# Kernel optimization log

Measured on AMD Instinct MI355X. Metric: run time of the kernel, lower is better.

Reference implementation:

```python
import jax, jax.numpy as jnp
import numpy as np

N = 50000   # nodes
E = 1600000 # edges
NF = 128    # input features
H = 128     # hidden
C = 40      # classes
EPS = 1e-5


def setup_inputs() -> dict:
    key = jax.random.key(0)
    ks = jax.random.split(key, 8)
    s_in = 1.0 / np.sqrt(NF)
    s_h = 1.0 / np.sqrt(H)
    return {
        "x": jax.random.normal(ks[0], (N, NF), jnp.float32),
        "edge_index": jax.random.randint(ks[1], (2, E), 0, N, dtype=jnp.int32),
        "W1": jax.random.normal(ks[2], (NF, H), jnp.float32) * s_in,
        "b1": jnp.zeros((H,), jnp.float32),
        "W2": jax.random.normal(ks[3], (H, H), jnp.float32) * s_h,
        "b2": jnp.zeros((H,), jnp.float32),
        "W3": jax.random.normal(ks[4], (H, H), jnp.float32) * s_h,
        "b3": jnp.zeros((H,), jnp.float32),
        "g1": jnp.ones((H,), jnp.float32), "be1": jnp.zeros((H,), jnp.float32),
        "g2": jnp.ones((H,), jnp.float32), "be2": jnp.zeros((H,), jnp.float32),
        "g3": jnp.ones((H,), jnp.float32), "be3": jnp.zeros((H,), jnp.float32),
        "fcW": jax.random.normal(ks[5], (H, C), jnp.float32) * s_h,
        "fcb": jnp.zeros((C,), jnp.float32),
    }


def _bn(x, g, b):
    # BatchNorm1d training-mode semantics: batch mean / biased batch var
    m = jnp.mean(x, axis=0)
    v = jnp.mean(jnp.square(x - m), axis=0)
    return g * (x - m) * jax.lax.rsqrt(v + EPS) + b


def reference(x, edge_index, W1, b1, W2, b2, W3, b3,
              g1, be1, g2, be2, g3, be3, fcW, fcb):
    n = x.shape[0]
    loop = jnp.arange(n, dtype=edge_index.dtype)
    src = jnp.concatenate([edge_index[0], loop])  # [E+N]
    dst = jnp.concatenate([edge_index[1], loop])
    # symmetric GCN normalization with self-loops
    deg = jax.ops.segment_sum(jnp.ones_like(src, dtype=x.dtype), dst, num_segments=n)
    dis = jnp.where(deg > 0, jax.lax.rsqrt(jnp.maximum(deg, 1.0)), 0.0)
    norm = dis[src] * dis[dst]  # [E+N]

    def conv(h, W, b):
        hw = h @ W  # [n, H]
        msg = hw[src] * norm[:, None]  # [E+N, H] gather + scale
        return jax.ops.segment_sum(msg, dst, num_segments=n) + b  # scatter-add

    h = jax.nn.relu(_bn(conv(x, W1, b1), g1, be1))
    h = jax.nn.relu(_bn(conv(h, W2, b2), g2, be2))  # dropout: eval mode (identity)
    h = jax.nn.relu(_bn(conv(h, W3, b3), g3, be3))
    logits = jax.nn.relu(h @ fcW + fcb)
    return jax.nn.log_softmax(logits, axis=1), logits
```

## Files before the change

### kernel.cpp

```cpp
#include <hip/hip_runtime.h>
#include <hip/hip_bf16.h>
#include <math.h>

#define NODES 50000
#define EDGES 1600000
#define HD    128
#define NC    40
#define EPSV  1e-5f
#define NBKT  196
#define CSRMAX 12032
#define NPART 32

typedef unsigned int uint;
typedef unsigned short ushort;
typedef __attribute__((ext_vector_type(8))) short bfrag;
typedef __attribute__((ext_vector_type(4))) float ffrag;

union FragU { uint4 u; bfrag f; };

__device__ inline ushort bf1(float x) {
  uint u = __float_as_uint(x);
  return (ushort)((u + 0x7fffu + ((u >> 16) & 1u)) >> 16);
}
__device__ inline uint bf2(float a, float b) {
  return (uint)bf1(a) | ((uint)bf1(b) << 16);
}
__device__ inline float ulo(uint u) { return __uint_as_float(u << 16); }
__device__ inline float uhi(uint u) { return __uint_as_float(u & 0xffff0000u); }

__global__ __launch_bounds__(256)
void k_bin_prepw(const int* __restrict__ src, const int* __restrict__ dst,
                 int* __restrict__ bcur, uint* __restrict__ staging, int e_,
                 const float* __restrict__ W1, const float* __restrict__ W2,
                 const float* __restrict__ W3, const float* __restrict__ fcW,
                 ushort* __restrict__ wt) {
  if (blockIdx.x >= 196) {
    int idx = (blockIdx.x - 196) * 256 + threadIdx.x;
    if (idx < 49152) {
      int r = idx >> 14;
      int i = idx & 16383;
      int nn = i >> 7, k = i & 127;
      const float* W = (r == 0) ? W1 : ((r == 1) ? W2 : W3);
      wt[idx] = bf1(W[k * 128 + nn]);
    } else if (idx < 55296) {
      int i = idx - 49152;
      int nn = i >> 7, k = i & 127;
      wt[idx] = (nn < NC) ? bf1(fcW[k * NC + nn]) : (ushort)0;
    }
    return;
  }
  __shared__ uint ent[8192];
  __shared__ int h[256], inc[256], lofs[256], cur[256], gb[256];
  int t = threadIdx.x;
  h[t] = 0;
  __syncthreads();
  int base = blockIdx.x * 8192;
  int cntE = min(8192, e_ - base);
  for (int i = t; i < cntE; i += 256) atomicAdd(&h[dst[base + i] >> 8], 1);
  __syncthreads();
  inc[t] = h[t];
  __syncthreads();
#pragma unroll
  for (int off = 1; off < 256; off <<= 1) {
    int y = (t >= off) ? inc[t - off] : 0;
    __syncthreads();
    inc[t] += y;
    __syncthreads();
  }
  lofs[t] = inc[t] - h[t];
  cur[t] = 0;
  __syncthreads();
  for (int i = t; i < cntE; i += 256) {
    int e = base + i;
    int d = dst[e];
    int b = d >> 8;
    uint en = (uint)(src[e] & 0xffff) | ((uint)(d & 255) << 16) | ((uint)b << 24);
    int p = lofs[b] + atomicAdd(&cur[b], 1);
    ent[p] = en;
  }
  __syncthreads();
  if (h[t]) gb[t] = atomicAdd(&bcur[t], h[t]);
  __syncthreads();
  for (int i = t; i < cntE; i += 256) {
    uint en = ent[i];
    int b = en >> 24;
    staging[(size_t)b * CSRMAX + gb[b] + (i - lofs[b])] = en;
  }
}

__global__ __launch_bounds__(256)
void k_csr(const uint* __restrict__ staging, const int* __restrict__ bcur,
           ushort* __restrict__ csr, int2* __restrict__ row_se,
           float* __restrict__ dis, int n) {
  __shared__ uint ent[CSRMAX];
  __shared__ ushort srt[CSRMAX];
  __shared__ int cnt_[256], ofs_[256], cur_[256];
  int b = blockIdx.x, t = threadIdx.x;
  size_t base = (size_t)b * CSRMAX;
  int cnt = min(bcur[b], CSRMAX);
  for (int i = t; i < cnt; i += 256) ent[i] = staging[base + i];
  cnt_[t] = 0;
  __syncthreads();
  for (int i = t; i < cnt; i += 256) atomicAdd(&cnt_[(ent[i] >> 16) & 255], 1);
  __syncthreads();
  ofs_[t] = cnt_[t];
  __syncthreads();
#pragma unroll
  for (int off = 1; off < 256; off <<= 1) {
    int y = (t >= off) ? ofs_[t - off] : 0;
    __syncthreads();
    ofs_[t] += y;
    __syncthreads();
  }
  int myofs = ofs_[t] - cnt_[t];
  ofs_[t] = myofs;
  cur_[t] = 0;
  __syncthreads();
  int node = (b << 8) + t;
  if (node < n) {
    row_se[node] = make_int2((int)base + myofs, (int)base + myofs + cnt_[t]);
    dis[node] = rsqrtf((float)(cnt_[t] + 1));
  }
  for (int i = t; i < cnt; i += 256) {
    uint e = ent[i];
    int dl = (e >> 16) & 255;
    int p = ofs_[dl] + atomicAdd(&cur_[dl], 1);
    srt[p] = (ushort)(e & 0xffff);
  }
  __syncthreads();
  for (int i = t; i < cnt; i += 256) csr[base + i] = srt[i];
}

__device__ inline void bn_prologue(const float* __restrict__ part,
                                   const float* __restrict__ g,
                                   const float* __restrict__ be,
                                   float* s_scale, float* s_shift) {
  __shared__ float tmp[256];
  int t = threadIdx.x;
  float s = 0.f;
#pragma unroll 8
  for (int p = 0; p < NPART; ++p) s += part[p * 256 + t];
  tmp[t] = s;
  __syncthreads();
  if (t < 128) {
    const float inv_n = 1.0f / (float)NODES;
    float m = tmp[t] * inv_n;
    float var = tmp[128 + t] * inv_n - m * m;
    float rstd = rsqrtf(var + EPSV);
    float sc = g[t] * rstd;
    s_scale[t] = sc;
    s_shift[t] = be[t] - m * sc;
  }
  __syncthreads();
}

template<int MODE>
__global__ __launch_bounds__(256)
void k_gemm_mx(const void* __restrict__ Ain, const uint* __restrict__ Wt,
               ushort* __restrict__ Cb, int n,
               const float* __restrict__ part, const float* __restrict__ g,
               const float* __restrict__ be) {
  __shared__ float s_scale[128], s_shift[128];
  if (MODE == 1) bn_prologue(part, g, be, s_scale, s_shift);

  const int lane = threadIdx.x & 63;
  const int wave = threadIdx.x >> 6;
  const int quad = lane >> 4;
  const int ml = lane & 15;
  const int row0 = blockIdx.x * 64 + wave * 16;
  const int arow = row0 + ml;
  ffrag acc[8];
#pragma unroll
  for (int i = 0; i < 8; ++i) acc[i] = (ffrag){0.f, 0.f, 0.f, 0.f};

#pragma unroll
  for (int s = 0; s < 4; ++s) {
    const int k0 = s * 32 + quad * 8;
    FragU a;
    if (arow < n) {
      if (MODE == 1) {
        const uint* Ab = (const uint*)Ain;
        uint4 v = *(const uint4*)&Ab[(size_t)arow * 64 + (k0 >> 1)];
        float4 sc0 = *(const float4*)&s_scale[k0];
        float4 sc1 = *(const float4*)&s_scale[k0 + 4];
        float4 sh0 = *(const float4*)&s_shift[k0];
        float4 sh1 = *(const float4*)&s_shift[k0 + 4];
        a.u.x = bf2(fmaxf(fmaf(ulo(v.x), sc0.x, sh0.x), 0.f), fmaxf(fmaf(uhi(v.x), sc0.y, sh0.y), 0.f));
        a.u.y = bf2(fmaxf(fmaf(ulo(v.y), sc0.z, sh0.z), 0.f), fmaxf(fmaf(uhi(v.y), sc0.w, sh0.w), 0.f));
        a.u.z = bf2(fmaxf(fmaf(ulo(v.z), sc1.x, sh1.x), 0.f), fmaxf(fmaf(uhi(v.z), sc1.y, sh1.y), 0.f));
        a.u.w = bf2(fmaxf(fmaf(ulo(v.w), sc1.z, sh1.z), 0.f), fmaxf(fmaf(uhi(v.w), sc1.w, sh1.w), 0.f));
      } else {
        const float* Af = (const float*)Ain;
        float4 a0 = *(const float4*)&Af[(size_t)arow * 128 + k0];
        float4 a1 = *(const float4*)&Af[(size_t)arow * 128 + k0 + 4];
        a.u.x = bf2(a0.x, a0.y);
        a.u.y = bf2(a0.z, a0.w);
        a.u.z = bf2(a1.x, a1.y);
        a.u.w = bf2(a1.z, a1.w);
      }
    } else {
      a.u = make_uint4(0, 0, 0, 0);
    }
#pragma unroll
    for (int nt = 0; nt < 8; ++nt) {
      FragU b;
      b.u = *(const uint4*)&Wt[(size_t)(nt * 16 + ml) * 64 + (k0 >> 1)];
      acc[nt] = __builtin_amdgcn_mfma_f32_16x16x32_bf16(a.f, b.f, acc[nt], 0, 0, 0);
    }
  }
#pragma unroll
  for (int nt = 0; nt < 8; ++nt) {
#pragma unroll
    for (int r = 0; r < 4; ++r) {
      int orow = row0 + quad * 4 + r;
      if (orow < n) Cb[(size_t)orow * 128 + nt * 16 + ml] = bf1(acc[nt][r]);
    }
  }
}

template<int FIRST>
__global__ __launch_bounds__(256)
void k_agg(const uint* __restrict__ t, const int2* __restrict__ row_se,
           const ushort* __restrict__ csr, uint* __restrict__ csrw,
           const float* __restrict__ dis,
           uint* __restrict__ hb, float* __restrict__ part, int n) {
  __shared__ float redS[4][128], redQ[4][128];
  int lane = threadIdx.x & 63;
  int wave = threadIdx.x >> 6;
  int quarter = lane >> 4;
  int fl = lane & 15;
  int node0 = blockIdx.x * 16 + wave * 4;
  float sS[8] = {}, sQ[8] = {};

  for (int ni = 0; ni < 4; ++ni) {
    int node = node0 + ni;
    int2 se = row_se[node];
    int e0 = se.x, e1 = se.y;
    float dd = dis[node];
    float acc[8] = {};
    for (int chunk = e0; chunk < e1; chunk += 64) {
      int m = min(64, e1 - chunk);
      uint ev = 0;
      if (lane < m) {
        if (FIRST) {
          int s = csr[chunk + lane];
          float w = dis[s] * dd;
          ev = (uint)s | ((uint)bf1(w) << 16);
          csrw[chunk + lane] = ev;
        } else {
          ev = csrw[chunk + lane];
        }
      }
#pragma unroll 2
      for (int j = 0; j < m; j += 8) {
        int j0 = j + quarter, j1 = j + 4 + quarter;
        uint ev0 = __shfl(ev, j0, 64);
        uint ev1 = __shfl(ev, j1, 64);
        bool p0 = j0 < m, p1 = j1 < m;
        uint4 v0 = make_uint4(0, 0, 0, 0), v1 = make_uint4(0, 0, 0, 0);
        if (p0) v0 = *(const uint4*)&t[(size_t)(ev0 & 0xffffu) * 64 + (fl << 2)];
        if (p1) v1 = *(const uint4*)&t[(size_t)(ev1 & 0xffffu) * 64 + (fl << 2)];
        float w0 = __uint_as_float(ev0 & 0xffff0000u);
        float w1 = __uint_as_float(ev1 & 0xffff0000u);
        if (p0) {
          acc[0] = fmaf(w0, ulo(v0.x), acc[0]); acc[1] = fmaf(w0, uhi(v0.x), acc[1]);
          acc[2] = fmaf(w0, ulo(v0.y), acc[2]); acc[3] = fmaf(w0, uhi(v0.y), acc[3]);
          acc[4] = fmaf(w0, ulo(v0.z), acc[4]); acc[5] = fmaf(w0, uhi(v0.z), acc[5]);
          acc[6] = fmaf(w0, ulo(v0.w), acc[6]); acc[7] = fmaf(w0, uhi(v0.w), acc[7]);
        }
        if (p1) {
          acc[0] = fmaf(w1, ulo(v1.x), acc[0]); acc[1] = fmaf(w1, uhi(v1.x), acc[1]);
          acc[2] = fmaf(w1, ulo(v1.y), acc[2]); acc[3] = fmaf(w1, uhi(v1.y), acc[3]);
          acc[4] = fmaf(w1, ulo(v1.z), acc[4]); acc[5] = fmaf(w1, uhi(v1.z), acc[5]);
          acc[6] = fmaf(w1, ulo(v1.w), acc[6]); acc[7] = fmaf(w1, uhi(v1.w), acc[7]);
        }
      }
    }
#pragma unroll
    for (int j = 0; j < 8; ++j) {
      acc[j] += __shfl_xor(acc[j], 16, 64);
      acc[j] += __shfl_xor(acc[j], 32, 64);
    }
    if (quarter == 0) {
      float d2 = dd * dd;
      uint4 v = *(const uint4*)&t[(size_t)node * 64 + (fl << 2)];
      acc[0] = fmaf(d2, ulo(v.x), acc[0]); acc[1] = fmaf(d2, uhi(v.x), acc[1]);
      acc[2] = fmaf(d2, ulo(v.y), acc[2]); acc[3] = fmaf(d2, uhi(v.y), acc[3]);
      acc[4] = fmaf(d2, ulo(v.z), acc[4]); acc[5] = fmaf(d2, uhi(v.z), acc[5]);
      acc[6] = fmaf(d2, ulo(v.w), acc[6]); acc[7] = fmaf(d2, uhi(v.w), acc[7]);
      uint4 o;
      o.x = bf2(acc[0], acc[1]);
      o.y = bf2(acc[2], acc[3]);
      o.z = bf2(acc[4], acc[5]);
      o.w = bf2(acc[6], acc[7]);
      *(uint4*)&hb[(size_t)node * 64 + (fl << 2)] = o;
#pragma unroll
      for (int j = 0; j < 8; ++j) {
        sS[j] += acc[j];
        sQ[j] += acc[j] * acc[j];
      }
    }
  }
  if (quarter == 0) {
#pragma unroll
    for (int j = 0; j < 8; ++j) {
      redS[wave][fl * 8 + j] = sS[j];
      redQ[wave][fl * 8 + j] = sQ[j];
    }
  }
  __syncthreads();
  int tt = threadIdx.x;
  if (tt < 128) {
    float s = redS[0][tt] + redS[1][tt] + redS[2][tt] + redS[3][tt];
    atomicAdd(&part[(blockIdx.x & (NPART - 1)) * 256 + tt], s);
  } else {
    int f = tt - 128;
    float s = redQ[0][f] + redQ[1][f] + redQ[2][f] + redQ[3][f];
    atomicAdd(&part[(blockIdx.x & (NPART - 1)) * 256 + tt], s);
  }
}

__global__ __launch_bounds__(256)
void k_fc_mx(const uint* __restrict__ hb, const float* __restrict__ part,
             const float* __restrict__ g, const float* __restrict__ be,
             const uint* __restrict__ fWt, const float* __restrict__ fcb,
             float* __restrict__ out, int n) {
  __shared__ float s_scale[128], s_shift[128];
  bn_prologue(part, g, be, s_scale, s_shift);

  const int lane = threadIdx.x & 63;
  const int wave = threadIdx.x >> 6;
  const int quad = lane >> 4;
  const int ml = lane & 15;
  const int row0 = blockIdx.x * 64 + wave * 16;
  const int arow = row0 + ml;
  ffrag acc[3];
#pragma unroll
  for (int i = 0; i < 3; ++i) acc[i] = (ffrag){0.f, 0.f, 0.f, 0.f};

#pragma unroll
  for (int s = 0; s < 4; ++s) {
    const int k0 = s * 32 + quad * 8;
    FragU a;
    if (arow < n) {
      uint4 v = *(const uint4*)&hb[(size_t)arow * 64 + (k0 >> 1)];
      float4 sc0 = *(const float4*)&s_scale[k0];
      float4 sc1 = *(const float4*)&s_scale[k0 + 4];
      float4 sh0 = *(const float4*)&s_shift[k0];
      float4 sh1 = *(const float4*)&s_shift[k0 + 4];
      a.u.x = bf2(fmaxf(fmaf(ulo(v.x), sc0.x, sh0.x), 0.f), fmaxf(fmaf(uhi(v.x), sc0.y, sh0.y), 0.f));
      a.u.y = bf2(fmaxf(fmaf(ulo(v.y), sc0.z, sh0.z), 0.f), fmaxf(fmaf(uhi(v.y), sc0.w, sh0.w), 0.f));
      a.u.z = bf2(fmaxf(fmaf(ulo(v.z), sc1.x, sh1.x), 0.f), fmaxf(fmaf(uhi(v.z), sc1.y, sh1.y), 0.f));
      a.u.w = bf2(fmaxf(fmaf(ulo(v.w), sc1.z, sh1.z), 0.f), fmaxf(fmaf(uhi(v.w), sc1.w, sh1.w), 0.f));
    } else {
      a.u = make_uint4(0, 0, 0, 0);
    }
#pragma unroll
    for (int nt = 0; nt < 3; ++nt) {
      FragU b;
      b.u = *(const uint4*)&fWt[(size_t)(nt * 16 + ml) * 64 + (k0 >> 1)];
      acc[nt] = __builtin_amdgcn_mfma_f32_16x16x32_bf16(a.f, b.f, acc[nt], 0, 0, 0);
    }
  }

  float b0 = fcb[ml], b1 = fcb[16 + ml];
  float b2 = (ml < 8) ? fcb[32 + ml] : 0.f;
#pragma unroll
  for (int r = 0; r < 4; ++r) {
    int orow = row0 + quad * 4 + r;
    if (orow >= n) continue;
    float l0 = fmaxf(acc[0][r] + b0, 0.f);
    float l1 = fmaxf(acc[1][r] + b1, 0.f);
    float l2 = (ml < 8) ? fmaxf(acc[2][r] + b2, 0.f) : -1e30f;
    float mx = fmaxf(fmaxf(l0, l1), l2);
#pragma unroll
    for (int off = 1; off < 16; off <<= 1) mx = fmaxf(mx, __shfl_xor(mx, off, 64));
    float sm = __expf(l0 - mx) + __expf(l1 - mx) + ((ml < 8) ? __expf(l2 - mx) : 0.f);
#pragma unroll
    for (int off = 1; off < 16; off <<= 1) sm += __shfl_xor(sm, off, 64);
    float lse = mx + __logf(sm);
    float* o1 = out + (size_t)orow * NC;
    float* o2 = out + (size_t)NODES * NC + (size_t)orow * NC;
    o1[ml] = l0 - lse;
    o1[16 + ml] = l1 - lse;
    o2[ml] = l0;
    o2[16 + ml] = l1;
    if (ml < 8) {
      o1[32 + ml] = l2 - lse;
      o2[32 + ml] = l2;
    }
  }
}


extern "C" void kernel_launch(void* const* d_in, const int* in_sizes, int n_in,
                              void* d_out, int out_size, void* d_ws, size_t ws_size,
                              hipStream_t stream) {
  (void)in_sizes; (void)n_in; (void)out_size; (void)ws_size;
  const float* x   = (const float*)d_in[0];
  const int*   ei  = (const int*)d_in[1];
  const float* W1  = (const float*)d_in[2];
  const float* W2  = (const float*)d_in[4];
  const float* W3  = (const float*)d_in[6];
  const float* g1  = (const float*)d_in[8];
  const float* be1 = (const float*)d_in[9];
  const float* g2  = (const float*)d_in[10];
  const float* be2 = (const float*)d_in[11];
  const float* g3  = (const float*)d_in[12];
  const float* be3 = (const float*)d_in[13];
  const float* fcW = (const float*)d_in[14];
  const float* fcb = (const float*)d_in[15];
  float* out = (float*)d_out;

  const int n = NODES, e_ = EDGES;
  const int* srcp = ei;
  const int* dstp = ei + e_;

  char* ws = (char*)d_ws;
  size_t off = 0;
  auto alloc = [&](size_t bytes) {
    char* p = ws + off;
    off = (off + bytes + 255) & ~(size_t)255;
    return p;
  };
  float* dis    = (float*)alloc((size_t)n * 4);
  int*   bcur   = (int*)  alloc(256 * 4);
  float* parts  = (float*)alloc(3 * NPART * 256 * 4);
  int2*  row_se = (int2*) alloc((size_t)n * 8);
  uint*  staging= (uint*) alloc((size_t)NBKT * CSRMAX * 4);
  ushort* csr   = (ushort*)alloc((size_t)NBKT * CSRMAX * 2);
  uint*  csrw   = (uint*) alloc((size_t)NBKT * CSRMAX * 4);
  uint*  tbuf   = (uint*) alloc((size_t)n * 64 * 4);
  uint*  hbuf   = (uint*) alloc((size_t)n * 64 * 4);
  ushort* wbuf  = (ushort*)alloc(55296 * 2);

  const uint* Wt1  = (const uint*)wbuf;
  const uint* Wt2  = (const uint*)wbuf + 8192;
  const uint* Wt3  = (const uint*)wbuf + 16384;
  const uint* fWt  = (const uint*)wbuf + 24576;

  hipMemsetAsync(bcur, 0, 256 * 4 + 3 * NPART * 256 * 4, stream);
  k_bin_prepw<<<196 + 216, 256, 0, stream>>>(srcp, dstp, bcur, staging, e_,
                                             W1, W2, W3, fcW, wbuf);
  k_csr<<<NBKT, 256, 0, stream>>>(staging, bcur, csr, row_se, dis, n);

  const int ggrid = (n + 63) / 64;
  const int agrid = n / 16;
  float* p0 = parts;
  float* p1 = parts + NPART * 256;
  float* p2 = parts + 2 * NPART * 256;

  k_gemm_mx<0><<<ggrid, 256, 0, stream>>>(x, Wt1, (ushort*)tbuf, n, nullptr, nullptr, nullptr);
  k_agg<1><<<agrid, 256, 0, stream>>>(tbuf, row_se, csr, csrw, dis, hbuf, p0, n);
  k_gemm_mx<1><<<ggrid, 256, 0, stream>>>(hbuf, Wt2, (ushort*)tbuf, n, p0, g1, be1);
  k_agg<0><<<agrid, 256, 0, stream>>>(tbuf, row_se, csr, csrw, dis, hbuf, p1, n);
  k_gemm_mx<1><<<ggrid, 256, 0, stream>>>(hbuf, Wt3, (ushort*)tbuf, n, p1, g2, be2);
  k_agg<0><<<agrid, 256, 0, stream>>>(tbuf, row_se, csr, csrw, dis, hbuf, p2, n);
  k_fc_mx<<<ggrid, 256, 0, stream>>>(hbuf, p2, g3, be3, fWt, fcb, out, n);
}
```

Baseline: 385.8 us.

## Fuse first-layer GEMM into CSR build kernel and compact CSR storage

The first feature GEMM (x @ W1) now runs as extra blocks of the CSR-building kernel, so the two independent jobs share one launch and can overlap. The CSR arrays are compacted to exactly E entries: each bucket computes its global offset with a prefix scan over bucket counts, replacing the padded per-bucket layout. Nontemporal loads and stores are added for the staging, csr and csrw streams. The cost is a redundant 256-element scan in every CSR block, plus a heavier combined kernel whose GEMM blocks may contend with the shared-memory-heavy CSR blocks.

```diff
diff --git a/kernel.cpp b/kernel.cpp
--- a/kernel.cpp
+++ b/kernel.cpp
@@ -10,6 +10,7 @@
 #define NBKT  196
 #define CSRMAX 12032
 #define NPART 32
+#define GT    782
 
 typedef unsigned int uint;
 typedef unsigned short ushort;
@@ -89,16 +90,72 @@
 }
 
 __global__ __launch_bounds__(256)
-void k_csr(const uint* __restrict__ staging, const int* __restrict__ bcur,
-           ushort* __restrict__ csr, int2* __restrict__ row_se,
-           float* __restrict__ dis, int n) {
+void k_csr_gemm0(const uint* __restrict__ staging, const int* __restrict__ bcur,
+                 ushort* __restrict__ csr, int2* __restrict__ row_se,
+                 float* __restrict__ dis, int n,
+                 const float* __restrict__ x, const uint* __restrict__ Wt,
+                 ushort* __restrict__ Cb) {
   __shared__ uint ent[CSRMAX];
   __shared__ ushort srt[CSRMAX];
-  __shared__ int cnt_[256], ofs_[256], cur_[256];
+  __shared__ int cnt_[256], ofs_[256], cur_[256], bsc[256];
+
+  if (blockIdx.x >= 196) {
+    const int lane = threadIdx.x & 63;
+    const int wave = threadIdx.x >> 6;
+    const int quad = lane >> 4;
+    const int ml = lane & 15;
+    const int row0 = (int)(blockIdx.x - 196) * 64 + wave * 16;
+    const int arow = row0 + ml;
+    ffrag acc[8];
+#pragma unroll
+    for (int i = 0; i < 8; ++i) acc[i] = (ffrag){0.f, 0.f, 0.f, 0.f};
+#pragma unroll
+    for (int s = 0; s < 4; ++s) {
+      const int k0 = s * 32 + quad * 8;
+      FragU a;
+      if (arow < n) {
+        float4 a0 = *(const float4*)&x[(size_t)arow * 128 + k0];
+        float4 a1 = *(const float4*)&x[(size_t)arow * 128 + k0 + 4];
+        a.u.x = bf2(a0.x, a0.y);
+        a.u.y = bf2(a0.z, a0.w);
+        a.u.z = bf2(a1.x, a1.y);
+        a.u.w = bf2(a1.z, a1.w);
+      } else {
+        a.u = make_uint4(0, 0, 0, 0);
+      }
+#pragma unroll
+      for (int nt = 0; nt < 8; ++nt) {
+        FragU b;
+        b.u = *(const uint4*)&Wt[(size_t)(nt * 16 + ml) * 64 + (k0 >> 1)];
+        acc[nt] = __builtin_amdgcn_mfma_f32_16x16x32_bf16(a.f, b.f, acc[nt], 0, 0, 0);
+      }
+    }
+#pragma unroll
+    for (int nt = 0; nt < 8; ++nt) {
+#pragma unroll
+      for (int r = 0; r < 4; ++r) {
+        int orow = row0 + quad * 4 + r;
+        if (orow < n) Cb[(size_t)orow * 128 + nt * 16 + ml] = bf1(acc[nt][r]);
+      }
+    }
+    return;
+  }
+
   int b = blockIdx.x, t = threadIdx.x;
-  size_t base = (size_t)b * CSRMAX;
+  int myc = min(bcur[t], CSRMAX);
+  bsc[t] = myc;
+  __syncthreads();
+#pragma unroll
+  for (int off = 1; off < 256; off <<= 1) {
+    int y = (t >= off) ? bsc[t - off] : 0;
+    __syncthreads();
+    bsc[t] += y;
+    __syncthreads();
+  }
+  int dbase = bsc[b] - min(bcur[b], CSRMAX);
+  size_t sbase = (size_t)b * CSRMAX;
   int cnt = min(bcur[b], CSRMAX);
-  for (int i = t; i < cnt; i += 256) ent[i] = staging[base + i];
+  for (int i = t; i < cnt; i += 256) ent[i] = __builtin_nontemporal_load(&staging[sbase + i]);
   cnt_[t] = 0;
   __syncthreads();
   for (int i = t; i < cnt; i += 256) atomicAdd(&cnt_[(ent[i] >> 16) & 255], 1);
@@ -118,7 +175,7 @@
   __syncthreads();
   int node = (b << 8) + t;
   if (node < n) {
-    row_se[node] = make_int2((int)base + myofs, (int)base + myofs + cnt_[t]);
+    row_se[node] = make_int2(dbase + myofs, dbase + myofs + cnt_[t]);
     dis[node] = rsqrtf((float)(cnt_[t] + 1));
   }
   for (int i = t; i < cnt; i += 256) {
@@ -128,7 +185,8 @@
     srt[p] = (ushort)(e & 0xffff);
   }
   __syncthreads();
-  for (int i = t; i < cnt; i += 256) csr[base + i] = srt[i];
+  for (int i = t; i < cnt; i += 256)
+    __builtin_nontemporal_store(srt[i], &csr[dbase + i]);
 }
 
 __device__ inline void bn_prologue(const float* __restrict__ part,
@@ -154,14 +212,13 @@
   __syncthreads();
 }
 
-template<int MODE>
 __global__ __launch_bounds__(256)
-void k_gemm_mx(const void* __restrict__ Ain, const uint* __restrict__ Wt,
+void k_gemm_mx(const uint* __restrict__ Ab, const uint* __restrict__ Wt,
                ushort* __restrict__ Cb, int n,
                const float* __restrict__ part, const float* __restrict__ g,
                const float* __restrict__ be) {
   __shared__ float s_scale[128], s_shift[128];
-  if (MODE == 1) bn_prologue(part, g, be, s_scale, s_shift);
+  bn_prologue(part, g, be, s_scale, s_shift);
 
   const int lane = threadIdx.x & 63;
   const int wave = threadIdx.x >> 6;
@@ -178,26 +235,15 @@
     const int k0 = s * 32 + quad * 8;
     FragU a;
     if (arow < n) {
-      if (MODE == 1) {
-        const uint* Ab = (const uint*)Ain;
-        uint4 v = *(const uint4*)&Ab[(size_t)arow * 64 + (k0 >> 1)];
-        float4 sc0 = *(const float4*)&s_scale[k0];
-        float4 sc1 = *(const float4*)&s_scale[k0 + 4];
-        float4 sh0 = *(const float4*)&s_shift[k0];
-        float4 sh1 = *(const float4*)&s_shift[k0 + 4];
-        a.u.x = bf2(fmaxf(fmaf(ulo(v.x), sc0.x, sh0.x), 0.f), fmaxf(fmaf(uhi(v.x), sc0.y, sh0.y), 0.f));
-        a.u.y = bf2(fmaxf(fmaf(ulo(v.y), sc0.z, sh0.z), 0.f), fmaxf(fmaf(uhi(v.y), sc0.w, sh0.w), 0.f));
-        a.u.z = bf2(fmaxf(fmaf(ulo(v.z), sc1.x, sh1.x), 0.f), fmaxf(fmaf(uhi(v.z), sc1.y, sh1.y), 0.f));
-        a.u.w = bf2(fmaxf(fmaf(ulo(v.w), sc1.z, sh1.z), 0.f), fmaxf(fmaf(uhi(v.w), sc1.w, sh1.w), 0.f));
-      } else {
-        const float* Af = (const float*)Ain;
-        float4 a0 = *(const float4*)&Af[(size_t)arow * 128 + k0];
-        float4 a1 = *(const float4*)&Af[(size_t)arow * 128 + k0 + 4];
-        a.u.x = bf2(a0.x, a0.y);
-        a.u.y = bf2(a0.z, a0.w);
-        a.u.z = bf2(a1.x, a1.y);
-        a.u.w = bf2(a1.z, a1.w);
-      }
+      uint4 v = *(const uint4*)&Ab[(size_t)arow * 64 + (k0 >> 1)];
+      float4 sc0 = *(const float4*)&s_scale[k0];
+      float4 sc1 = *(const float4*)&s_scale[k0 + 4];
+      float4 sh0 = *(const float4*)&s_shift[k0];
+      float4 sh1 = *(const float4*)&s_shift[k0 + 4];
+      a.u.x = bf2(fmaxf(fmaf(ulo(v.x), sc0.x, sh0.x), 0.f), fmaxf(fmaf(uhi(v.x), sc0.y, sh0.y), 0.f));
+      a.u.y = bf2(fmaxf(fmaf(ulo(v.y), sc0.z, sh0.z), 0.f), fmaxf(fmaf(uhi(v.y), sc0.w, sh0.w), 0.f));
+      a.u.z = bf2(fmaxf(fmaf(ulo(v.z), sc1.x, sh1.x), 0.f), fmaxf(fmaf(uhi(v.z), sc1.y, sh1.y), 0.f));
+      a.u.w = bf2(fmaxf(fmaf(ulo(v.w), sc1.z, sh1.z), 0.f), fmaxf(fmaf(uhi(v.w), sc1.w, sh1.w), 0.f));
     } else {
       a.u = make_uint4(0, 0, 0, 0);
     }
@@ -243,12 +289,12 @@
       uint ev = 0;
       if (lane < m) {
         if (FIRST) {
-          int s = csr[chunk + lane];
+          int s = __builtin_nontemporal_load(&csr[chunk + lane]);
           float w = dis[s] * dd;
           ev = (uint)s | ((uint)bf1(w) << 16);
-          csrw[chunk + lane] = ev;
+          __builtin_nontemporal_store(ev, &csrw[chunk + lane]);
         } else {
-          ev = csrw[chunk + lane];
+          ev = __builtin_nontemporal_load(&csrw[chunk + lane]);
         }
       }
 #pragma unroll 2
@@ -428,8 +474,8 @@
   float* parts  = (float*)alloc(3 * NPART * 256 * 4);
   int2*  row_se = (int2*) alloc((size_t)n * 8);
   uint*  staging= (uint*) alloc((size_t)NBKT * CSRMAX * 4);
-  ushort* csr   = (ushort*)alloc((size_t)NBKT * CSRMAX * 2);
-  uint*  csrw   = (uint*) alloc((size_t)NBKT * CSRMAX * 4);
+  ushort* csr   = (ushort*)alloc((size_t)e_ * 2);
+  uint*  csrw   = (uint*) alloc((size_t)e_ * 4);
   uint*  tbuf   = (uint*) alloc((size_t)n * 64 * 4);
   uint*  hbuf   = (uint*) alloc((size_t)n * 64 * 4);
   ushort* wbuf  = (ushort*)alloc(55296 * 2);
@@ -442,19 +488,18 @@
   hipMemsetAsync(bcur, 0, 256 * 4 + 3 * NPART * 256 * 4, stream);
   k_bin_prepw<<<196 + 216, 256, 0, stream>>>(srcp, dstp, bcur, staging, e_,
                                              W1, W2, W3, fcW, wbuf);
-  k_csr<<<NBKT, 256, 0, stream>>>(staging, bcur, csr, row_se, dis, n);
-
-  const int ggrid = (n + 63) / 64;
+  k_csr_gemm0<<<196 + GT, 256, 0, stream>>>(staging, bcur, csr, row_se, dis, n,
+                                            x, Wt1, (ushort*)tbuf);
+
   const int agrid = n / 16;
   float* p0 = parts;
   float* p1 = parts + NPART * 256;
   float* p2 = parts + 2 * NPART * 256;
 
-  k_gemm_mx<0><<<ggrid, 256, 0, stream>>>(x, Wt1, (ushort*)tbuf, n, nullptr, nullptr, nullptr);
   k_agg<1><<<agrid, 256, 0, stream>>>(tbuf, row_se, csr, csrw, dis, hbuf, p0, n);
-  k_gemm_mx<1><<<ggrid, 256, 0, stream>>>(hbuf, Wt2, (ushort*)tbuf, n, p0, g1, be1);
+  k_gemm_mx<<<GT, 256, 0, stream>>>(hbuf, Wt2, (ushort*)tbuf, n, p0, g1, be1);
   k_agg<0><<<agrid, 256, 0, stream>>>(tbuf, row_se, csr, csrw, dis, hbuf, p1, n);
-  k_gemm_mx<1><<<ggrid, 256, 0, stream>>>(hbuf, Wt3, (ushort*)tbuf, n, p1, g2, be2);
+  k_gemm_mx<<<GT, 256, 0, stream>>>(hbuf, Wt3, (ushort*)tbuf, n, p1, g2, be2);
   k_agg<0><<<agrid, 256, 0, stream>>>(tbuf, row_se, csr, csrw, dis, hbuf, p2, n);
-  k_fc_mx<<<ggrid, 256, 0, stream>>>(hbuf, p2, g3, be3, fWt, fcb, out, n);
-}
+  k_fc_mx<<<GT, 256, 0, stream>>>(hbuf, p2, g3, be3, fWt, fcb, out, n);
+}
```

New measurement: 383.8 us. Within noise of the previous version (-0.5%).
